# Kernel tuning notes

Hardware: AMD Instinct MI355X
Metric: run time of the kernel (lower is better)

## Reference

```python
import jax, jax.numpy as jnp
import numpy as np

E = 1024  # embedding == hidden size
L = 2     # layer_num
S = 128   # sentence_length == seq_len
B = 64
LABEL = 5


def setup_inputs() -> dict:
    key = jax.random.key(0)
    ks = jax.random.split(key, 20)
    sc = 1.0 / np.sqrt(2 * E)
    def lin(k, i, o):
        kw, kb = jax.random.split(k)
        return (jax.random.uniform(kw, (i, o), jnp.float32, -sc, sc),
                jax.random.uniform(kb, (o,), jnp.float32, -sc, sc))
    # per-direction stacked gate weights [L, 2E, E]
    def gates(k):
        kk = jax.random.split(k, 3 * L)
        Ws, bs = [], []
        for g in range(3):
            W = jnp.stack([lin(kk[g * L + l], 2 * E, E)[0] for l in range(L)])
            b = jnp.stack([lin(jax.random.fold_in(kk[g * L + l], 7), 2 * E, E)[1] for l in range(L)])
            Ws.append(W); bs.append(b)
        return Ws, bs
    (fW, fb) = gates(ks[0])
    (bW, bb) = gates(ks[1])
    word_W, word_b = lin(ks[2], 2 * E, 1)
    pw = 1.0 / np.sqrt(S)
    pred_W = jax.random.uniform(ks[3], (S, LABEL), jnp.float32, -pw, pw)
    pred_b = jax.random.uniform(ks[4], (LABEL,), jnp.float32, -pw, pw)
    return {
        "inputs": jax.random.normal(ks[5], (B, S, E), jnp.float32),
        "cell_states": jnp.zeros((B, E), jnp.float32),
        "hidden_states": jnp.zeros((B, E), jnp.float32),
        "back_states": jnp.zeros((B, E), jnp.float32),
        "back_hidden": jnp.zeros((B, E), jnp.float32),
        "fWf": fW[0], "fbf": fb[0], "fWi": fW[1], "fbi": fb[1], "fWc": fW[2], "fbc": fb[2],
        "bWf": bW[0], "bbf": bb[0], "bWi": bW[1], "bbi": bb[1], "bWc": bW[2], "bbc": bb[2],
        "word_W": word_W, "word_b": word_b, "pred_W": pred_W, "pred_b": pred_b,
    }


def _run_dir(x_seq, h0, c0, Wf, bf, Wi, bi, Wc, bc):
    # x_seq: [S,B,E]; h0,c0: [B,E] broadcast to all layers
    hc0 = (jnp.broadcast_to(h0, (L,) + h0.shape), jnp.broadcast_to(c0, (L,) + c0.shape))
    def step(carry, x_t):
        h, c = carry
        inp = x_t
        hs, cs = [], []
        for l in range(L):
            z = jnp.concatenate([h[l], inp], axis=-1)       # [B,2E]
            f = jax.nn.sigmoid(z @ Wf[l] + bf[l])
            i = jax.nn.sigmoid(z @ Wi[l] + bi[l])
            g = jnp.tanh(z @ Wc[l] + bc[l])
            c_new = c[l] * f + i * g
            h_new = jnp.tanh(c_new) * f                     # note: forget gate reused as output gate (as in source)
            hs.append(h_new); cs.append(c_new); inp = h_new
        return (jnp.stack(hs), jnp.stack(cs)), inp
    _, out = jax.lax.scan(step, hc0, x_seq)
    return out  # [S,B,E]


def reference(inputs, cell_states, hidden_states, back_states, back_hidden,
              fWf, fbf, fWi, fbi, fWc, fbc,
              bWf, bbf, bWi, bbi, bWc, bbc,
              word_W, word_b, pred_W, pred_b):
    x = jnp.transpose(inputs, (1, 0, 2))                     # [S,B,E]
    fwd = _run_dir(x, hidden_states, cell_states, fWf, fbf, fWi, fbi, fWc, fbc)
    bwd = _run_dir(x[::-1], hidden_states, cell_states, bWf, bbf, bWi, bbi, bWc, bbc)[::-1]
    out = jnp.concatenate([fwd, bwd], axis=-1)               # [S,B,2E]
    out = jnp.transpose(out, (1, 0, 2))                      # [B,S,2E]
    w = (out @ word_W + word_b).reshape(out.shape[0], -1)    # [B,S]
    return w @ pred_W + pred_b                               # [B,LABEL]
```

## Files before the change

### kernel.cpp

```cpp
#include <hip/hip_runtime.h>
#include <cstddef>
#include <cstdint>

typedef _Float16 half8 __attribute__((ext_vector_type(8)));
typedef float f32x4 __attribute__((ext_vector_type(4)));

#define S_LEN 128
#define B_SZ  64
#define E_SZ  1024
#define NLBL  5
#define NPHASE 129

#define WOFF_WREC  0ull
#define WOFF_WINP  25165824ull
#define WOFF_X16   50331648ull
#define M0_H0    67108864ull
#define M0_H1    100925440ull
#define M0_WPART 134742016ull
#define M0_W     138936320ull
#define M0_FLAGS 138969088ull
#define NEED0    139001856ull
#define M1_H0    67108864ull
#define M1_H1    67633152ull
#define M1_WPART 68157440ull
#define M1_W     72351744ull
#define M1_FLAGS 72384512ull
#define NEED1    72417280ull

struct PP {
  const float* x;
  const float* W[2][3];
  const float* bias[2][3];
  const float* wordW;
  const float* cs0;
  _Float16* wrec;
  _Float16* winp;
  _Float16* x16;
  _Float16* h0;
  _Float16* h1;
  float* w;
  float* wpart;
  int* flags;
};

__device__ __forceinline__ uint32_t pack2f16(float a, float b) {
  return (uint32_t)__builtin_bit_cast(unsigned short, (_Float16)a) |
         ((uint32_t)__builtin_bit_cast(unsigned short, (_Float16)b) << 16);
}

#define MFMA16(A, B, C) __builtin_amdgcn_mfma_f32_16x16x32_f16(A, B, C, 0, 0, 0)

#define S_ISSUE_A4C(Q, P0, P1, P2, P3)                                     \
  asm volatile("global_load_dwordx4 %0, %4, off sc0 sc1\n\t"               \
               "global_load_dwordx4 %1, %5, off sc0 sc1\n\t"               \
               "global_load_dwordx4 %2, %6, off sc0 sc1\n\t"               \
               "global_load_dwordx4 %3, %7, off sc0 sc1"                   \
               : "=&v"((Q)[0]), "=&v"((Q)[1]), "=&v"((Q)[2]), "=&v"((Q)[3]) \
               : "v"(P0), "v"(P1), "v"(P2), "v"(P3))

#define S_ISSUE_A4P(Q, P0, P1, P2, P3)                                     \
  asm volatile("global_load_dwordx4 %0, %4, off\n\t"                       \
               "global_load_dwordx4 %1, %5, off\n\t"                       \
               "global_load_dwordx4 %2, %6, off\n\t"                       \
               "global_load_dwordx4 %3, %7, off"                           \
               : "=&v"((Q)[0]), "=&v"((Q)[1]), "=&v"((Q)[2]), "=&v"((Q)[3]) \
               : "v"(P0), "v"(P1), "v"(P2), "v"(P3))

#define S_ISSUE_W6(Q, P0, P1, P2, P3, P4, P5)                              \
  asm volatile("global_load_dwordx4 %0, %6, off\n\t"                       \
               "global_load_dwordx4 %1, %7, off\n\t"                       \
               "global_load_dwordx4 %2, %8, off\n\t"                       \
               "global_load_dwordx4 %3, %9, off\n\t"                       \
               "global_load_dwordx4 %4, %10, off\n\t"                      \
               "global_load_dwordx4 %5, %11, off"                          \
               : "=&v"((Q)[0]), "=&v"((Q)[1]), "=&v"((Q)[2]), "=&v"((Q)[3]), \
                 "=&v"((Q)[4]), "=&v"((Q)[5])                              \
               : "v"(P0), "v"(P1), "v"(P2), "v"(P3), "v"(P4), "v"(P5))

#define S_WAITV(N)                                                         \
  asm volatile("s_waitcnt vmcnt(" #N ")" ::: "memory");                    \
  __builtin_amdgcn_sched_barrier(0)

__device__ __forceinline__ void comp_rec2s(const uint4* q, int kcA,
                                           const _Float16* wlds, int l64,
                                           f32x4 acc[3][2]) {
  #pragma unroll
  for (int s = 0; s < 2; ++s) {
    const int kc = kcA + s;
    const half8 a0 = __builtin_bit_cast(half8, q[s * 2 + 0]);
    const half8 a1 = __builtin_bit_cast(half8, q[s * 2 + 1]);
    #pragma unroll
    for (int g = 0; g < 3; ++g) {
      const half8 bf = *(const half8*)(wlds + ((size_t)(g * 32 + kc) * 64 + l64) * 8);
      acc[g][0] = MFMA16(a0, bf, acc[g][0]);
      acc[g][1] = MFMA16(a1, bf, acc[g][1]);
    }
  }
}

__device__ __forceinline__ void comp_inp2(const uint4* aq, const uint4* wq,
                                          f32x4 acc[3][2]) {
  #pragma unroll
  for (int s = 0; s < 2; ++s) {
    const half8 a0 = __builtin_bit_cast(half8, aq[s * 2 + 0]);
    const half8 a1 = __builtin_bit_cast(half8, aq[s * 2 + 1]);
    #pragma unroll
    for (int g = 0; g < 3; ++g) {
      const half8 bf = __builtin_bit_cast(half8, wq[s * 3 + g]);
      acc[g][0] = MFMA16(a0, bf, acc[g][0]);
      acc[g][1] = MFMA16(a1, bf, acc[g][1]);
    }
  }
}

__global__ __launch_bounds__(256)
void conv_w_kernel(PP p) {
  const int blk = blockIdx.x;
  const int part = blk & 1;
  const int j16 = (blk >> 1) & 63;
  const int rest = blk >> 7;
  const int g = rest % 3;
  const int dl = rest / 3;
  const int l = dl & 1, d = dl >> 1;
  const int tid = threadIdx.x;
  const int l2 = tid & 63, kc0 = tid >> 6;
  const float* W = p.W[d][g] + (size_t)l * 2048 * 1024 + (size_t)(part ? 1024 : 0) * 1024;
  _Float16* out = (part ? p.winp : p.wrec) + (size_t)(dl * 64 + j16) * 49152 + (size_t)g * 16384;
  const int j = j16 * 16 + (l2 & 15);
  const int kbase = (l2 >> 4) * 8;
  #pragma unroll
  for (int ki = 0; ki < 8; ++ki) {
    const int kc = kc0 * 8 + ki;
    const int k0 = kc * 32 + kbase;
    half8 h;
    #pragma unroll
    for (int e2 = 0; e2 < 8; ++e2) h[e2] = (_Float16)W[(size_t)(k0 + e2) * 1024 + j];
    *(half8*)(out + ((size_t)kc * 64 + l2) * 8) = h;
  }
}

__global__ __launch_bounds__(256)
void conv_x_kernel(const float* x, _Float16* x16) {
  const size_t i8 = ((size_t)blockIdx.x * 256 + threadIdx.x) * 8;
  float4 a = *(const float4*)(x + i8);
  float4 b = *(const float4*)(x + i8 + 4);
  half8 h;
  h[0] = (_Float16)a.x; h[1] = (_Float16)a.y; h[2] = (_Float16)a.z; h[3] = (_Float16)a.w;
  h[4] = (_Float16)b.x; h[5] = (_Float16)b.y; h[6] = (_Float16)b.z; h[7] = (_Float16)b.w;
  *(half8*)(x16 + i8) = h;
}

template<int MODE>
__global__ __launch_bounds__(256)
void init2_kernel(PP p, const float* hs) {
  const size_t HU = (MODE == 0) ? 65536 : 131072;
  const size_t i = (size_t)blockIdx.x * 256 + threadIdx.x;
  if (i < 2 * HU) {
    const size_t ai = (i < HU) ? i : i - HU;
    _Float16* dst = (i < HU) ? p.h0 : p.h1;
    const size_t grp = ai >> 15;
    const size_t be = ai & 32767;
    const size_t b = be >> 9, ec = be & 511;
    const uint32_t v = pack2f16(hs[b * 1024 + ec * 2], hs[b * 1024 + ec * 2 + 1]);
    const size_t u32off = (MODE == 0) ? (grp * 129 * 32768 + be) : (grp * 32768 + be);
    ((uint32_t*)dst)[u32off] = v;
  } else if (i < 2 * HU + 8192) {
    p.flags[i - 2 * HU] = 0;
  }
}

template<int MODE>
__global__ __launch_bounds__(512, 2)
void lstm_persist(PP p) {
  extern __shared__ char smem[];
  _Float16* wlds = (_Float16*)smem;
  float* pre  = (float*)(smem + 98304);
  float* wred = (float*)(smem + 153600);

  const int tid = threadIdx.x;
  const int l64 = tid & 63, lr = l64 & 15, lg = l64 >> 4;
  const int wv = tid >> 6, kq = wv & 3, mg = wv >> 2;
  const int blk = blockIdx.x;
  const int j16 = blk & 63, l = (blk >> 6) & 1, d = blk >> 7;
  const int idx = blk & 127;
  const int j0 = j16 * 16;

  if (tid == 0)
    (void)__hip_atomic_load(p.flags, __ATOMIC_ACQUIRE, __HIP_MEMORY_SCOPE_AGENT);
  __syncthreads();

  const size_t tileoff = (size_t)((d * 2 + l) * 64 + j16) * 49152;
  {
    const float4* src = (const float4*)(p.wrec + tileoff);
    float4* dst = (float4*)wlds;
    #pragma unroll
    for (int i = 0; i < 12; ++i) dst[tid + i * 512] = src[tid + i * 512];
  }
  const _Float16* wtile = p.winp + tileoff;
  _Float16* hrec_arr = l ? p.h1 : p.h0;

  const int pr = tid >> 3;
  const int pj = (tid & 7) * 2;
  const int pjg = j0 + pj;
  const float bsf0 = p.bias[d][0][l * E_SZ + pjg], bsf1 = p.bias[d][0][l * E_SZ + pjg + 1];
  const float bsi0 = p.bias[d][1][l * E_SZ + pjg], bsi1 = p.bias[d][1][l * E_SZ + pjg + 1];
  const float bsc0 = p.bias[d][2][l * E_SZ + pjg], bsc1 = p.bias[d][2][l * E_SZ + pjg + 1];
  const float ww0 = p.wordW[d * E_SZ + pjg], ww1 = p.wordW[d * E_SZ + pjg + 1];
  float creg0 = p.cs0[(size_t)pr * E_SZ + pjg];
  float creg1 = p.cs0[(size_t)pr * E_SZ + pjg + 1];
  __syncthreads();

  auto hoff = [&](int dd, int s) -> size_t {
    return (MODE == 0) ? ((size_t)dd * 129 + s) * 65536 : ((size_t)(dd * 2 + s)) * 65536;
  };

  for (int ph = 0; ph < NPHASE; ++ph) {
    const int t = l ? (ph - 1) : ph;
    if ((unsigned)t < (unsigned)S_LEN) {
      const int par = t & 1, prev = par ^ 1;
      const int td = d ? (S_LEN - 1 - t) : t;
      const int rs    = (MODE == 0) ? t : prev;
      const int wslot = (MODE == 0) ? (t + 1) : par;
      const int islot = (MODE == 0) ? (t + 1) : par;

      const _Float16* hAf = hrec_arr + hoff(d, rs);
      const _Float16* r0 = hAf + (size_t)(mg * 32 + lr) * 1024;
      const _Float16* r1 = hAf + (size_t)(mg * 32 + 16 + lr) * 1024;
      const _Float16* a0base;
      const _Float16* a1base;
      if (l == 0) {
        a0base = p.x16 + ((size_t)(mg * 32 + lr) * S_LEN + td) * 1024;
        a1base = p.x16 + ((size_t)(mg * 32 + 16 + lr) * S_LEN + td) * 1024;
      } else {
        const _Float16* hf = p.h0 + hoff(d, islot);
        a0base = hf + (size_t)(mg * 32 + lr) * 1024;
        a1base = hf + (size_t)(mg * 32 + 16 + lr) * 1024;
      }

      const f32x4 zero = {0.f, 0.f, 0.f, 0.f};
      f32x4 acc[3][2];
      #pragma unroll
      for (int g = 0; g < 3; ++g) { acc[g][0] = zero; acc[g][1] = zero; }

      auto issue_rec = [&](int c, uint4* Q) {
        const int kk = (kq * 8 + c * 2) * 32 + lg * 8;
        if (MODE == 0) {
          S_ISSUE_A4P(Q, r0 + kk, r1 + kk, r0 + kk + 32, r1 + kk + 32);
        } else {
          S_ISSUE_A4C(Q, r0 + kk, r1 + kk, r0 + kk + 32, r1 + kk + 32);
        }
      };
      auto issue_a = [&](int c, uint4* Q) {
        const int kk = (kq * 8 + c * 2) * 32 + lg * 8;
        if (MODE == 0 || l == 0) {
          S_ISSUE_A4P(Q, a0base + kk, a1base + kk, a0base + kk + 32, a1base + kk + 32);
        } else {
          S_ISSUE_A4C(Q, a0base + kk, a1base + kk, a0base + kk + 32, a1base + kk + 32);
        }
      };
      auto issue_w = [&](int c, uint4* Q) {
        const int kc0 = kq * 8 + c * 2;
        S_ISSUE_W6(Q,
                   wtile + ((size_t)(0 * 32 + kc0) * 64 + l64) * 8,
                   wtile + ((size_t)(1 * 32 + kc0) * 64 + l64) * 8,
                   wtile + ((size_t)(2 * 32 + kc0) * 64 + l64) * 8,
                   wtile + ((size_t)(0 * 32 + kc0 + 1) * 64 + l64) * 8,
                   wtile + ((size_t)(1 * 32 + kc0 + 1) * 64 + l64) * 8,
                   wtile + ((size_t)(2 * 32 + kc0 + 1) * 64 + l64) * 8);
      };

      uint4 rq[2][4], aq[2][4], wq[2][6];
      issue_rec(0, rq[0]);
      issue_rec(1, rq[1]); S_WAITV(4);  comp_rec2s(rq[0], kq * 8 + 0, wlds, l64, acc);
      issue_rec(2, rq[0]); S_WAITV(4);  comp_rec2s(rq[1], kq * 8 + 2, wlds, l64, acc);
      issue_rec(3, rq[1]); S_WAITV(4);  comp_rec2s(rq[0], kq * 8 + 4, wlds, l64, acc);
      issue_a(0, aq[0]); issue_w(0, wq[0]);
      S_WAITV(10);                      comp_rec2s(rq[1], kq * 8 + 6, wlds, l64, acc);
      issue_a(1, aq[1]); issue_w(1, wq[1]);
      S_WAITV(10);                      comp_inp2(aq[0], wq[0], acc);
      issue_a(2, aq[0]); issue_w(2, wq[0]);
      S_WAITV(10);                      comp_inp2(aq[1], wq[1], acc);
      issue_a(3, aq[1]); issue_w(3, wq[1]);
      S_WAITV(10);                      comp_inp2(aq[0], wq[0], acc);
      S_WAITV(0);                       comp_inp2(aq[1], wq[1], acc);

      #pragma unroll
      for (int g = 0; g < 3; ++g)
        #pragma unroll
        for (int mt = 0; mt < 2; ++mt)
          #pragma unroll
          for (int pp = 0; pp < 4; ++pp)
            pre[(((kq * 3 + g) * 64) + (mg * 2 + mt) * 16 + lg * 4 + pp) * 18 + lr] =
                acc[g][mt][pp];
      __syncthreads();

      float fp0 = bsf0, fp1 = bsf1, ip0 = bsi0, ip1 = bsi1, cp0 = bsc0, cp1 = bsc1;
      #pragma unroll
      for (int k = 0; k < 4; ++k) {
        fp0 += pre[((k * 3 + 0) * 64 + pr) * 18 + pj];
        fp1 += pre[((k * 3 + 0) * 64 + pr) * 18 + pj + 1];
        ip0 += pre[((k * 3 + 1) * 64 + pr) * 18 + pj];
        ip1 += pre[((k * 3 + 1) * 64 + pr) * 18 + pj + 1];
        cp0 += pre[((k * 3 + 2) * 64 + pr) * 18 + pj];
        cp1 += pre[((k * 3 + 2) * 64 + pr) * 18 + pj + 1];
      }
      const float fg0 = 1.f / (1.f + expf(-fp0)), fg1 = 1.f / (1.f + expf(-fp1));
      const float ig0 = 1.f / (1.f + expf(-ip0)), ig1 = 1.f / (1.f + expf(-ip1));
      const float gg0 = tanhf(cp0), gg1 = tanhf(cp1);
      creg0 = creg0 * fg0 + ig0 * gg0;
      creg1 = creg1 * fg1 + ig1 * gg1;
      const float h0v = tanhf(creg0) * fg0;
      const float h1v = tanhf(creg1) * fg1;

      uint32_t* hdst = (uint32_t*)(hrec_arr + hoff(d, wslot) + (size_t)pr * 1024 + pjg);
      const uint32_t pk = pack2f16(h0v, h1v);
      asm volatile("global_store_dword %0, %1, off sc0 sc1" ::"v"(hdst), "v"(pk) : "memory");
      if (l) {
        wred[pr * 16 + pj] = h0v * ww0;
        wred[pr * 16 + pj + 1] = h1v * ww1;
        __syncthreads();
        if (tid < 64) {
          float s = 0.f;
          #pragma unroll
          for (int q = 0; q < 16; ++q) s += wred[tid * 16 + q];
          p.wpart[((size_t)(d * 64 + j16) * S_LEN + td) * 64 + tid] = s;
        }
      }
    }

    __syncthreads();
    if (tid == 0) {
      __hip_atomic_store(p.flags + (size_t)(d * 128 + idx) * 32, ph + 1,
                         __ATOMIC_RELAXED, __HIP_MEMORY_SCOPE_AGENT);
      asm volatile("s_waitcnt vmcnt(0)" ::: "memory");
    }
    if (tid < 128) {
      const int* fl = p.flags + (size_t)(d * 128 + tid) * 32;
      int f, it = 0;
      do {
        f = __hip_atomic_load(fl, __ATOMIC_RELAXED, __HIP_MEMORY_SCOPE_AGENT);
        if (f >= ph + 1) break;
        __builtin_amdgcn_s_sleep(1);
      } while (++it < (1 << 22));
    }
    __syncthreads();
  }
}

__global__ __launch_bounds__(64)
void reduce_w_kernel(const float* wpart, const float* wordb, float* w) {
  const int t = blockIdx.x, b = threadIdx.x;
  float s = wordb[0];
  #pragma unroll 8
  for (int q = 0; q < 128; ++q)
    s += wpart[((size_t)q * S_LEN + t) * 64 + b];
  w[b * S_LEN + t] = s;
}

__global__ __launch_bounds__(320)
void final_kernel(const float* w, const float* predW, const float* predb, float* out) {
  const int tid = threadIdx.x;
  if (tid >= B_SZ * NLBL) return;
  const int b = tid / NLBL, lab = tid % NLBL;
  float s = predb[lab];
  #pragma unroll 8
  for (int t = 0; t < S_LEN; ++t) s += w[b * S_LEN + t] * predW[t * NLBL + lab];
  out[tid] = s;
}

extern "C" void kernel_launch(void* const* d_in, const int* in_sizes, int n_in,
                              void* d_out, int out_size, void* d_ws, size_t ws_size,
                              hipStream_t stream) {
  char* ws = (char*)d_ws;
  const bool hist = (ws_size >= NEED0);

  PP p;
  p.x = (const float*)d_in[0];
  p.W[0][0] = (const float*)d_in[5];  p.bias[0][0] = (const float*)d_in[6];
  p.W[0][1] = (const float*)d_in[7];  p.bias[0][1] = (const float*)d_in[8];
  p.W[0][2] = (const float*)d_in[9];  p.bias[0][2] = (const float*)d_in[10];
  p.W[1][0] = (const float*)d_in[11]; p.bias[1][0] = (const float*)d_in[12];
  p.W[1][1] = (const float*)d_in[13]; p.bias[1][1] = (const float*)d_in[14];
  p.W[1][2] = (const float*)d_in[15]; p.bias[1][2] = (const float*)d_in[16];
  p.wordW = (const float*)d_in[17];
  p.cs0   = (const float*)d_in[1];
  p.wrec  = (_Float16*)(ws + WOFF_WREC);
  p.winp  = (_Float16*)(ws + WOFF_WINP);
  p.x16   = (_Float16*)(ws + WOFF_X16);
  if (hist) {
    p.h0    = (_Float16*)(ws + M0_H0);
    p.h1    = (_Float16*)(ws + M0_H1);
    p.wpart = (float*)(ws + M0_WPART);
    p.w     = (float*)(ws + M0_W);
    p.flags = (int*)(ws + M0_FLAGS);
  } else {
    p.h0    = (_Float16*)(ws + M1_H0);
    p.h1    = (_Float16*)(ws + M1_H1);
    p.wpart = (float*)(ws + M1_WPART);
    p.w     = (float*)(ws + M1_W);
    p.flags = (int*)(ws + M1_FLAGS);
  }

  hipFuncSetAttribute(reinterpret_cast<const void*>(&lstm_persist<0>),
                      hipFuncAttributeMaxDynamicSharedMemorySize, 157696);
  hipFuncSetAttribute(reinterpret_cast<const void*>(&lstm_persist<1>),
                      hipFuncAttributeMaxDynamicSharedMemorySize, 157696);

  conv_w_kernel<<<1536, 256, 0, stream>>>(p);
  conv_x_kernel<<<4096, 256, 0, stream>>>(p.x, p.x16);
  if (hist) {
    init2_kernel<0><<<544, 256, 0, stream>>>(p, (const float*)d_in[2]);
    lstm_persist<0><<<256, 512, 157696, stream>>>(p);
  } else {
    init2_kernel<1><<<1056, 256, 0, stream>>>(p, (const float*)d_in[2]);
    lstm_persist<1><<<256, 512, 157696, stream>>>(p);
  }
  reduce_w_kernel<<<128, 64, 0, stream>>>(p.wpart, (const float*)d_in[18], p.w);
  final_kernel<<<1, 320, 0, stream>>>(p.w, (const float*)d_in[19],
                                      (const float*)d_in[20], (float*)d_out);
}
```

Measured before the change: 1.530 ms.

## Keep input-projection weights in registers and reschedule the per-step load pipeline

The input-weight tile slice each wave needs (24 uint4 per lane) is loaded once into registers before the time loop, instead of being re-fetched from global memory every phase. The per-step load pipeline is restructured into a three-buffer rotation that now carries only the recurrent-state and input-activation loads. The padding stride of the partial-sum LDS buffer drops from 18 to 17 floats, which shrinks shared memory and may change bank conflicts. Holding 96 extra VGPRs per lane risks register spills at 2 blocks of 512 threads per CU.

```diff
diff --git a/kernel.cpp b/kernel.cpp
--- a/kernel.cpp
+++ b/kernel.cpp
@@ -65,17 +65,6 @@
                "global_load_dwordx4 %3, %7, off"                           \
                : "=&v"((Q)[0]), "=&v"((Q)[1]), "=&v"((Q)[2]), "=&v"((Q)[3]) \
                : "v"(P0), "v"(P1), "v"(P2), "v"(P3))
-
-#define S_ISSUE_W6(Q, P0, P1, P2, P3, P4, P5)                              \
-  asm volatile("global_load_dwordx4 %0, %6, off\n\t"                       \
-               "global_load_dwordx4 %1, %7, off\n\t"                       \
-               "global_load_dwordx4 %2, %8, off\n\t"                       \
-               "global_load_dwordx4 %3, %9, off\n\t"                       \
-               "global_load_dwordx4 %4, %10, off\n\t"                      \
-               "global_load_dwordx4 %5, %11, off"                          \
-               : "=&v"((Q)[0]), "=&v"((Q)[1]), "=&v"((Q)[2]), "=&v"((Q)[3]), \
-                 "=&v"((Q)[4]), "=&v"((Q)[5])                              \
-               : "v"(P0), "v"(P1), "v"(P2), "v"(P3), "v"(P4), "v"(P5))
 
 #define S_WAITV(N)                                                         \
   asm volatile("s_waitcnt vmcnt(" #N ")" ::: "memory");                    \
@@ -175,7 +164,7 @@
   extern __shared__ char smem[];
   _Float16* wlds = (_Float16*)smem;
   float* pre  = (float*)(smem + 98304);
-  float* wred = (float*)(smem + 153600);
+  float* wred = (float*)(smem + 150528);
 
   const int tid = threadIdx.x;
   const int l64 = tid & 63, lr = l64 & 15, lg = l64 >> 4;
@@ -198,6 +187,14 @@
   }
   const _Float16* wtile = p.winp + tileoff;
   _Float16* hrec_arr = l ? p.h1 : p.h0;
+
+  uint4 wreg[24];
+  #pragma unroll
+  for (int i = 0; i < 24; ++i) {
+    const int kcl = i / 3, g = i % 3;
+    const int kc = kq * 8 + kcl;
+    wreg[i] = *(const uint4*)(wtile + ((size_t)(g * 32 + kc) * 64 + l64) * 8);
+  }
 
   const int pr = tid >> 3;
   const int pj = (tid & 7) * 2;
@@ -258,31 +255,17 @@
           S_ISSUE_A4C(Q, a0base + kk, a1base + kk, a0base + kk + 32, a1base + kk + 32);
         }
       };
-      auto issue_w = [&](int c, uint4* Q) {
-        const int kc0 = kq * 8 + c * 2;
-        S_ISSUE_W6(Q,
-                   wtile + ((size_t)(0 * 32 + kc0) * 64 + l64) * 8,
-                   wtile + ((size_t)(1 * 32 + kc0) * 64 + l64) * 8,
-                   wtile + ((size_t)(2 * 32 + kc0) * 64 + l64) * 8,
-                   wtile + ((size_t)(0 * 32 + kc0 + 1) * 64 + l64) * 8,
-                   wtile + ((size_t)(1 * 32 + kc0 + 1) * 64 + l64) * 8,
-                   wtile + ((size_t)(2 * 32 + kc0 + 1) * 64 + l64) * 8);
-      };
-
-      uint4 rq[2][4], aq[2][4], wq[2][6];
-      issue_rec(0, rq[0]);
-      issue_rec(1, rq[1]); S_WAITV(4);  comp_rec2s(rq[0], kq * 8 + 0, wlds, l64, acc);
-      issue_rec(2, rq[0]); S_WAITV(4);  comp_rec2s(rq[1], kq * 8 + 2, wlds, l64, acc);
-      issue_rec(3, rq[1]); S_WAITV(4);  comp_rec2s(rq[0], kq * 8 + 4, wlds, l64, acc);
-      issue_a(0, aq[0]); issue_w(0, wq[0]);
-      S_WAITV(10);                      comp_rec2s(rq[1], kq * 8 + 6, wlds, l64, acc);
-      issue_a(1, aq[1]); issue_w(1, wq[1]);
-      S_WAITV(10);                      comp_inp2(aq[0], wq[0], acc);
-      issue_a(2, aq[0]); issue_w(2, wq[0]);
-      S_WAITV(10);                      comp_inp2(aq[1], wq[1], acc);
-      issue_a(3, aq[1]); issue_w(3, wq[1]);
-      S_WAITV(10);                      comp_inp2(aq[0], wq[0], acc);
-      S_WAITV(0);                       comp_inp2(aq[1], wq[1], acc);
+
+      uint4 b0[4], b1[4], b2[4];
+      issue_rec(0, b0); issue_rec(1, b1); issue_rec(2, b2);
+      S_WAITV(8); comp_rec2s(b0, kq * 8 + 0, wlds, l64, acc); issue_rec(3, b0);
+      S_WAITV(8); comp_rec2s(b1, kq * 8 + 2, wlds, l64, acc); issue_a(0, b1);
+      S_WAITV(8); comp_rec2s(b2, kq * 8 + 4, wlds, l64, acc); issue_a(1, b2);
+      S_WAITV(8); comp_rec2s(b0, kq * 8 + 6, wlds, l64, acc); issue_a(2, b0);
+      S_WAITV(8); comp_inp2(b1, &wreg[0],  acc); issue_a(3, b1);
+      S_WAITV(8); comp_inp2(b2, &wreg[6],  acc);
+      S_WAITV(4); comp_inp2(b0, &wreg[12], acc);
+      S_WAITV(0); comp_inp2(b1, &wreg[18], acc);
 
       #pragma unroll
       for (int g = 0; g < 3; ++g)
@@ -290,19 +273,19 @@
         for (int mt = 0; mt < 2; ++mt)
           #pragma unroll
           for (int pp = 0; pp < 4; ++pp)
-            pre[(((kq * 3 + g) * 64) + (mg * 2 + mt) * 16 + lg * 4 + pp) * 18 + lr] =
+            pre[(((kq * 3 + g) * 64) + (mg * 2 + mt) * 16 + lg * 4 + pp) * 17 + lr] =
                 acc[g][mt][pp];
       __syncthreads();
 
       float fp0 = bsf0, fp1 = bsf1, ip0 = bsi0, ip1 = bsi1, cp0 = bsc0, cp1 = bsc1;
       #pragma unroll
       for (int k = 0; k < 4; ++k) {
-        fp0 += pre[((k * 3 + 0) * 64 + pr) * 18 + pj];
-        fp1 += pre[((k * 3 + 0) * 64 + pr) * 18 + pj + 1];
-        ip0 += pre[((k * 3 + 1) * 64 + pr) * 18 + pj];
-        ip1 += pre[((k * 3 + 1) * 64 + pr) * 18 + pj + 1];
-        cp0 += pre[((k * 3 + 2) * 64 + pr) * 18 + pj];
-        cp1 += pre[((k * 3 + 2) * 64 + pr) * 18 + pj + 1];
+        fp0 += pre[((k * 3 + 0) * 64 + pr) * 17 + pj];
+        fp1 += pre[((k * 3 + 0) * 64 + pr) * 17 + pj + 1];
+        ip0 += pre[((k * 3 + 1) * 64 + pr) * 17 + pj];
+        ip1 += pre[((k * 3 + 1) * 64 + pr) * 17 + pj + 1];
+        cp0 += pre[((k * 3 + 2) * 64 + pr) * 17 + pj];
+        cp1 += pre[((k * 3 + 2) * 64 + pr) * 17 + pj + 1];
       }
       const float fg0 = 1.f / (1.f + expf(-fp0)), fg1 = 1.f / (1.f + expf(-fp1));
       const float ig0 = 1.f / (1.f + expf(-ip0)), ig1 = 1.f / (1.f + expf(-ip1));
@@ -402,18 +385,18 @@
   }
 
   hipFuncSetAttribute(reinterpret_cast<const void*>(&lstm_persist<0>),
-                      hipFuncAttributeMaxDynamicSharedMemorySize, 157696);
+                      hipFuncAttributeMaxDynamicSharedMemorySize, 155648);
   hipFuncSetAttribute(reinterpret_cast<const void*>(&lstm_persist<1>),
-                      hipFuncAttributeMaxDynamicSharedMemorySize, 157696);
+                      hipFuncAttributeMaxDynamicSharedMemorySize, 155648);
 
   conv_w_kernel<<<1536, 256, 0, stream>>>(p);
   conv_x_kernel<<<4096, 256, 0, stream>>>(p.x, p.x16);
   if (hist) {
     init2_kernel<0><<<544, 256, 0, stream>>>(p, (const float*)d_in[2]);
-    lstm_persist<0><<<256, 512, 157696, stream>>>(p);
+    lstm_persist<0><<<256, 512, 155648, stream>>>(p);
   } else {
     init2_kernel<1><<<1056, 256, 0, stream>>>(p, (const float*)d_in[2]);
-    lstm_persist<1><<<256, 512, 157696, stream>>>(p);
+    lstm_persist<1><<<256, 512, 155648, stream>>>(p);
   }
   reduce_w_kernel<<<128, 64, 0, stream>>>(p.wpart, (const float*)d_in[18], p.w);
   final_kernel<<<1, 320, 0, stream>>>(p.w, (const float*)d_in[19],
```

Result: faster. 1.360 ms (-11.1%).
